# Performance work log

Measured on AMD Instinct MI355X. Metric: run time of the kernel, lower is better.

## Reference

```python
import jax, jax.numpy as jnp
import numpy as np

DURATION = 100.0   # init kwarg: duration
RESOLUTION = 0.1   # init kwarg: resolution
OUT_LEN = int(DURATION / RESOLUTION) + 1  # 1001


def setup_inputs() -> dict:
    key = jax.random.key(0)
    k1, k2 = jax.random.split(key)
    B, S, D = 32, 4096, 256
    embed_batch = jax.random.normal(k1, (B, S, D), dtype=jnp.float32)
    # sorted timestamps spanning [0, DURATION]
    ts_batch = jnp.sort(jax.random.uniform(k2, (B, S), dtype=jnp.float32) * DURATION, axis=-1)
    return {"embed_batch": embed_batch, "ts_batch": ts_batch}


def reference(embed_batch, ts_batch):
    # embed_batch: [B, S, D], ts_batch: [B, S] (sorted along last dim)
    B, S, D = embed_batch.shape
    ts_new = jnp.linspace(0.0, DURATION, OUT_LEN).astype(embed_batch.dtype)  # [L]
    # batched searchsorted replaces the per-sample/per-channel Python loops
    idx = jax.vmap(lambda t: jnp.searchsorted(t, ts_new))(ts_batch)  # [B, L]
    idx = jnp.clip(idx, 1, S - 1)
    lo = idx - 1  # [B, L]
    hi = idx
    x_lo = jnp.take_along_axis(ts_batch, lo, axis=1)  # [B, L]
    x_hi = jnp.take_along_axis(ts_batch, hi, axis=1)
    y_lo = jnp.take_along_axis(embed_batch, lo[:, :, None], axis=1)  # [B, L, D]
    y_hi = jnp.take_along_axis(embed_batch, hi[:, :, None], axis=1)
    slope = (y_hi - y_lo) / (x_hi - x_lo)[:, :, None]
    y_new = slope * (ts_new[None, :, None] - x_lo[:, :, None]) + y_lo
    return y_new  # [B, OUT_LEN, D]
```

## Files before the change

### kernel.cpp

```cpp
#include <hip/hip_runtime.h>


#define RS_B 32
#define RS_S 4096
#define RS_D 256
#define RS_OUTLEN 1001
#define RS_PPW 16

__global__ __launch_bounds__(64) void resample_kernel(
    const float* __restrict__ embed,
    const float* __restrict__ ts,
    float* __restrict__ out)
{
    const int b  = blockIdx.y;
    const int l0 = blockIdx.x * RS_PPW;
    const int lane = threadIdx.x;
    const int p = lane & 15;

    int l = l0 + p;
    if (l > RS_OUTLEN - 1) l = RS_OUTLEN - 1;
    const float t = (float)((double)l * (100.0 / 1000.0));

    const float* __restrict__ tsr = ts + (size_t)b * RS_S;

    int lo = 0, hi = RS_S;
#pragma unroll
    for (int it = 0; it < 12; ++it) {
        int mid = (lo + hi) >> 1;
        float v = tsr[mid];
        if (v < t) lo = mid + 1; else hi = mid;
    }
    int idx = lo;
    if (idx < 1) idx = 1;
    if (idx > RS_S - 1) idx = RS_S - 1;

    const float x_lo = tsr[idx - 1];
    const float x_hi = tsr[idx];
    const float w1 = (t - x_lo) / (x_hi - x_lo);

    const float4* __restrict__ ebase =
        (const float4*)(embed + (size_t)b * RS_S * RS_D);
    float4* __restrict__ obase =
        (float4*)(out + ((size_t)b * RS_OUTLEN + (size_t)l0) * RS_D);

#pragma unroll
    for (int q = 0; q < RS_PPW; ++q) {
        if (l0 + q > RS_OUTLEN - 1) break;
        const int   sidx = __shfl(idx, q);
        const float sw   = __shfl(w1,  q);

        const float4* plo = ebase + (size_t)(sidx - 1) * (RS_D / 4) + lane;
        const float4* phi = plo + (RS_D / 4);
        float4 a = *plo;
        float4 c = *phi;
        float4 r;
        r.x = a.x + (c.x - a.x) * sw;
        r.y = a.y + (c.y - a.y) * sw;
        r.z = a.z + (c.z - a.z) * sw;
        r.w = a.w + (c.w - a.w) * sw;
        *(obase + (size_t)q * (RS_D / 4) + lane) = r;
    }
}

extern "C" void kernel_launch(void* const* d_in, const int* in_sizes, int n_in,
                              void* d_out, int out_size, void* d_ws, size_t ws_size,
                              hipStream_t stream) {
    const float* embed = (const float*)d_in[0];
    const float* ts    = (const float*)d_in[1];
    float* out         = (float*)d_out;

    dim3 grid((RS_OUTLEN + RS_PPW - 1) / RS_PPW, RS_B);
    resample_kernel<<<grid, 64, 0, stream>>>(embed, ts, out);
}
```

Measured before the change: 22.05 us.

## Halve points per workgroup, remap workgroups across XCDs, use nontemporal loads/stores

Each workgroup now handles 8 output points instead of 16, which doubles the number of workgroups for more parallelism. A 1D grid is remapped so that consecutive workgroup IDs, which are dispatched round-robin across the 8 XCDs, land on contiguous batch/position tiles. The embedding loads and output stores switch to nontemporal builtins on ext_vector types to reduce cache pollution. The cost is that each workgroup still runs a full binary search, so more workgroups means more of that per-workgroup overhead. Nontemporal loads may also lose reuse, since neighbouring output points often read the same embedding rows.

```diff
diff --git a/kernel.cpp b/kernel.cpp
--- a/kernel.cpp
+++ b/kernel.cpp
@@ -5,17 +5,24 @@
 #define RS_S 4096
 #define RS_D 256
 #define RS_OUTLEN 1001
-#define RS_PPW 16
+#define RS_PPW 8
+#define RS_NBX ((RS_OUTLEN + RS_PPW - 1) / RS_PPW)
+#define RS_NWG (RS_NBX * RS_B)
+
+typedef float f32x4 __attribute__((ext_vector_type(4)));
 
 __global__ __launch_bounds__(64) void resample_kernel(
     const float* __restrict__ embed,
     const float* __restrict__ ts,
     float* __restrict__ out)
 {
-    const int b  = blockIdx.y;
-    const int l0 = blockIdx.x * RS_PPW;
+    const int lin = blockIdx.x;
+    const int wg  = (lin & 7) * (RS_NWG / 8) + (lin >> 3);
+    const int b   = wg / RS_NBX;
+    const int l0  = (wg - b * RS_NBX) * RS_PPW;
+
     const int lane = threadIdx.x;
-    const int p = lane & 15;
+    const int p = lane & (RS_PPW - 1);
 
     int l = l0 + p;
     if (l > RS_OUTLEN - 1) l = RS_OUTLEN - 1;
@@ -38,10 +45,10 @@
     const float x_hi = tsr[idx];
     const float w1 = (t - x_lo) / (x_hi - x_lo);
 
-    const float4* __restrict__ ebase =
-        (const float4*)(embed + (size_t)b * RS_S * RS_D);
-    float4* __restrict__ obase =
-        (float4*)(out + ((size_t)b * RS_OUTLEN + (size_t)l0) * RS_D);
+    const f32x4* __restrict__ ebase =
+        (const f32x4*)(embed + (size_t)b * RS_S * RS_D);
+    f32x4* __restrict__ obase =
+        (f32x4*)(out + ((size_t)b * RS_OUTLEN + (size_t)l0) * RS_D);
 
 #pragma unroll
     for (int q = 0; q < RS_PPW; ++q) {
@@ -49,16 +56,12 @@
         const int   sidx = __shfl(idx, q);
         const float sw   = __shfl(w1,  q);
 
-        const float4* plo = ebase + (size_t)(sidx - 1) * (RS_D / 4) + lane;
-        const float4* phi = plo + (RS_D / 4);
-        float4 a = *plo;
-        float4 c = *phi;
-        float4 r;
-        r.x = a.x + (c.x - a.x) * sw;
-        r.y = a.y + (c.y - a.y) * sw;
-        r.z = a.z + (c.z - a.z) * sw;
-        r.w = a.w + (c.w - a.w) * sw;
-        *(obase + (size_t)q * (RS_D / 4) + lane) = r;
+        const f32x4* plo = ebase + (size_t)(sidx - 1) * (RS_D / 4) + lane;
+        const f32x4* phi = plo + (RS_D / 4);
+        f32x4 a = __builtin_nontemporal_load(plo);
+        f32x4 c = __builtin_nontemporal_load(phi);
+        f32x4 r = a + (c - a) * sw;
+        __builtin_nontemporal_store(r, obase + (size_t)q * (RS_D / 4) + lane);
     }
 }
 
@@ -69,6 +72,5 @@
     const float* ts    = (const float*)d_in[1];
     float* out         = (float*)d_out;
 
-    dim3 grid((RS_OUTLEN + RS_PPW - 1) / RS_PPW, RS_B);
-    resample_kernel<<<grid, 64, 0, stream>>>(embed, ts, out);
+    resample_kernel<<<RS_NWG, 64, 0, stream>>>(embed, ts, out);
 }
```

Measured after the change: 22.28 us. About the same (+1.1%).
